# Performance work log

Measured on AMD Instinct MI355X. Metric: run time of the kernel, lower is better.

## Reference

```python
import jax, jax.numpy as jnp
import numpy as np

EPS = 1e-6  # config.model.train_hparams.eps
DIM_MODEL = 512
DIM_K = 64  # dim_q = dim_k = dim_v


def setup_inputs() -> dict:
    key = jax.random.key(0)
    ks = jax.random.split(key, 10)
    B, S = 8, 2048
    query = jax.random.normal(ks[0], (B, S, DIM_MODEL), dtype=jnp.float32)
    key_t = jax.random.normal(ks[1], (B, S, DIM_MODEL), dtype=jnp.float32)
    value = jax.random.normal(ks[2], (B, S, DIM_MODEL), dtype=jnp.float32)
    attention_mask = jax.random.randint(ks[3], (B, S, S), 0, 2, dtype=jnp.int32)
    lim = 1.0 / np.sqrt(DIM_MODEL)
    Wq = jax.random.uniform(ks[4], (DIM_K, DIM_MODEL), jnp.float32, -lim, lim)
    bq = jax.random.uniform(ks[5], (DIM_K,), jnp.float32, -lim, lim)
    Wk = jax.random.uniform(ks[6], (DIM_K, DIM_MODEL), jnp.float32, -lim, lim)
    bk = jax.random.uniform(ks[7], (DIM_K,), jnp.float32, -lim, lim)
    Wv = jax.random.uniform(ks[8], (DIM_K, DIM_MODEL), jnp.float32, -lim, lim)
    bv = jax.random.uniform(ks[9], (DIM_K,), jnp.float32, -lim, lim)
    return {"query": query, "key": key_t, "value": value,
            "attention_mask": attention_mask,
            "Wq": Wq, "bq": bq, "Wk": Wk, "bk": bk, "Wv": Wv, "bv": bv}


def reference(query, key, value, attention_mask, Wq, bq, Wk, bk, Wv, bv):
    scale = DIM_K ** (-0.5)
    q = jnp.einsum('bsm,dm->bsd', query, Wq) + bq   # (B,S,dk)
    k = jnp.einsum('bsm,dm->bsd', key, Wk) + bk
    v = jnp.einsum('bsm,dm->bsd', value, Wv) + bv
    qk = jnp.einsum('bqd,bkd->bqk', q, k) * scale   # (B,S,S)
    qk = jnp.where(qk == 0, EPS, qk)                 # masked_fill(qk == 0, eps)
    qk = jnp.where(attention_mask == 0, EPS, qk)     # masked_fill(mask == 0, eps)
    attention_weight = jax.nn.softmax(qk, axis=-1)
    attention = jnp.einsum('bqk,bkd->bqd', attention_weight, v)
    return attention, attention_weight
```

## Files before the change

### kernel.cpp

```cpp
#include <hip/hip_runtime.h>

#define BATCH 8
#define SEQ   2048
#define DM    512
#define DK    64
#define NROW  (BATCH*SEQ)
#define EPSV  1e-6f

typedef _Float16 f16x8 __attribute__((ext_vector_type(8)));
typedef _Float16 f16x4 __attribute__((ext_vector_type(4)));
typedef _Float16 f16x2 __attribute__((ext_vector_type(2)));
typedef float    f32x4 __attribute__((ext_vector_type(4)));

__global__ void wcvt(const float* __restrict__ wq, const float* __restrict__ wk,
                     const float* __restrict__ wv, _Float16* __restrict__ w16) {
    int idx = (blockIdx.x * 256 + threadIdx.x) * 4;
    int z = idx >> 15;
    int off = idx & 32767;
    const float* src = (z == 0) ? wq : ((z == 1) ? wk : wv);
    float4 g = *reinterpret_cast<const float4*>(src + off);
    f16x4 h = { (_Float16)g.x, (_Float16)g.y, (_Float16)g.z, (_Float16)g.w };
    *reinterpret_cast<f16x4*>(w16 + idx) = h;
}

__global__ __launch_bounds__(256) void proj(
    const float* __restrict__ query, const float* __restrict__ key,
    const float* __restrict__ value, const _Float16* __restrict__ w16,
    const float* __restrict__ bq, const float* __restrict__ bk, const float* __restrict__ bv,
    _Float16* __restrict__ q16, _Float16* __restrict__ k16, _Float16* __restrict__ vT16)
{
    __shared__ _Float16 xsh[64][72];

    const int t = threadIdx.x;
    const int wave = t >> 6, lane = t & 63;
    const int n16 = lane & 15, quad = lane >> 4;
    const int z = blockIdx.y;
    const float* in   = (z == 0) ? query : ((z == 1) ? key : value);
    const float* bias = (z == 0) ? bq    : ((z == 1) ? bk  : bv);
    const _Float16* wz = w16 + z * (DK * DM);
    const int row0 = blockIdx.x * 64;

    f32x4 acc[4] = {};

    for (int kk = 0; kk < DM; kk += 64) {
        #pragma unroll
        for (int it = 0; it < 4; ++it) {
            int f = t + it * 256;
            int row = f >> 4, kq = f & 15;
            float4 g = *reinterpret_cast<const float4*>(in + (size_t)(row0 + row) * DM + kk + kq * 4);
            f16x4 h = { (_Float16)g.x, (_Float16)g.y, (_Float16)g.z, (_Float16)g.w };
            *reinterpret_cast<f16x4*>(&xsh[row][kq * 4]) = h;
        }
        __syncthreads();
        f16x8 a0 = *reinterpret_cast<const f16x8*>(&xsh[wave * 16 + n16][quad * 8]);
        f16x8 a1 = *reinterpret_cast<const f16x8*>(&xsh[wave * 16 + n16][32 + quad * 8]);
        #pragma unroll
        for (int nt = 0; nt < 4; ++nt) {
            const _Float16* bbase = wz + (size_t)(nt * 16 + n16) * DM + kk + quad * 8;
            f16x8 b0 = *reinterpret_cast<const f16x8*>(bbase);
            f16x8 b1 = *reinterpret_cast<const f16x8*>(bbase + 32);
            acc[nt] = __builtin_amdgcn_mfma_f32_16x16x32_f16(a0, b0, acc[nt], 0, 0, 0);
            acc[nt] = __builtin_amdgcn_mfma_f32_16x16x32_f16(a1, b1, acc[nt], 0, 0, 0);
        }
        __syncthreads();
    }

    const int batch = row0 >> 11, row0s = row0 & (SEQ - 1);
    if (z < 2) {
        _Float16* out = (z == 0) ? q16 : k16;
        #pragma unroll
        for (int nt = 0; nt < 4; ++nt) {
            float bzv = bias[nt * 16 + n16];
            #pragma unroll
            for (int r = 0; r < 4; ++r) {
                int grow = row0 + wave * 16 + quad * 4 + r;
                out[(size_t)grow * DK + nt * 16 + n16] = (_Float16)(acc[nt][r] + bzv);
            }
        }
    } else {
        #pragma unroll
        for (int nt = 0; nt < 4; ++nt) {
            float bzv = bias[nt * 16 + n16];
            f16x4 h = { (_Float16)(acc[nt][0] + bzv), (_Float16)(acc[nt][1] + bzv),
                        (_Float16)(acc[nt][2] + bzv), (_Float16)(acc[nt][3] + bzv) };
            int d = nt * 16 + n16;
            int sbase = row0s + wave * 16 + quad * 4;
            *reinterpret_cast<f16x4*>(vT16 + ((size_t)(batch * DK + d)) * SEQ + sbase) = h;
        }
    }
}

#define RTILE 8
#define SCP   2064

__global__ __launch_bounds__(256, 2) void attn(
    const _Float16* __restrict__ q16,
    const _Float16* __restrict__ k16,
    const _Float16* __restrict__ vT16,
    const int* __restrict__ mask,
    float* __restrict__ attno,
    float* __restrict__ aw)
{
    __shared__ float sc[RTILE][SCP];
    __shared__ _Float16 psh[16][72];
    __shared__ float st_il[RTILE];

    const int t = threadIdx.x;
    const int wave = t >> 6, lane = t & 63;
    const int n16 = lane & 15, quad = lane >> 4;
    const int row0 = blockIdx.x * RTILE;
    const int batch = row0 >> 11, row0s = row0 & (SEQ - 1);

    for (int i = t; i < 16 * 36; i += 256) ((float*)psh)[i] = 0.0f;

    {
        const _Float16* qb = q16 + (size_t)(row0 + n16) * DK + quad * 8;
        f16x8 aq0 = *reinterpret_cast<const f16x8*>(qb);
        f16x8 aq1 = *reinterpret_cast<const f16x8*>(qb + 32);
        for (int c = 0; c < 32; ++c) {
            int key = c * 64 + wave * 16 + n16;
            const _Float16* kb = k16 + (size_t)(batch * SEQ + key) * DK + quad * 8;
            f16x8 b0 = *reinterpret_cast<const f16x8*>(kb);
            f16x8 b1 = *reinterpret_cast<const f16x8*>(kb + 32);
            f32x4 acc = {};
            acc = __builtin_amdgcn_mfma_f32_16x16x32_f16(aq0, b0, acc, 0, 0, 0);
            acc = __builtin_amdgcn_mfma_f32_16x16x32_f16(aq1, b1, acc, 0, 0, 0);
            if (quad < 2) {
                int col = c * 64 + wave * 16 + n16;
                #pragma unroll
                for (int r = 0; r < 4; ++r)
                    sc[quad * 4 + r][col] = acc[r] * 0.125f;
            }
        }
    }
    __syncthreads();

    #pragma unroll
    for (int rr = 0; rr < 2; ++rr) {
        int row = wave * 2 + rr;
        const int4* mrow = reinterpret_cast<const int4*>(
            mask + (size_t)batch * SEQ * SEQ + (size_t)(row0s + row) * SEQ);
        float vmax = -3.4e38f;
        #pragma unroll
        for (int it = 0; it < 8; ++it) {
            int j = it * 64 + lane;
            int4  m4 = mrow[j];
            float4 s4 = *reinterpret_cast<float4*>(&sc[row][j * 4]);
            s4.x = (m4.x == 0 || s4.x == 0.0f) ? EPSV : s4.x;
            s4.y = (m4.y == 0 || s4.y == 0.0f) ? EPSV : s4.y;
            s4.z = (m4.z == 0 || s4.z == 0.0f) ? EPSV : s4.z;
            s4.w = (m4.w == 0 || s4.w == 0.0f) ? EPSV : s4.w;
            *reinterpret_cast<float4*>(&sc[row][j * 4]) = s4;
            vmax = fmaxf(vmax, fmaxf(fmaxf(s4.x, s4.y), fmaxf(s4.z, s4.w)));
        }
        #pragma unroll
        for (int off = 32; off; off >>= 1) vmax = fmaxf(vmax, __shfl_xor(vmax, off));
        float vsum = 0.0f;
        #pragma unroll
        for (int it = 0; it < 8; ++it) {
            int j = it * 64 + lane;
            float4 s4 = *reinterpret_cast<float4*>(&sc[row][j * 4]);
            float4 e4 = { __expf(s4.x - vmax), __expf(s4.y - vmax),
                          __expf(s4.z - vmax), __expf(s4.w - vmax) };
            *reinterpret_cast<float4*>(&sc[row][j * 4]) = e4;
            vsum += (e4.x + e4.y) + (e4.z + e4.w);
        }
        #pragma unroll
        for (int off = 32; off; off >>= 1) vsum += __shfl_xor(vsum, off);
        if (lane == 0) st_il[row] = 1.0f / vsum;
    }
    __syncthreads();

    f32x4 oacc = {};
    const int rowp = t >> 5;
    const int col2 = (t & 31) * 2;
    const float il = st_il[rowp];
    float* awrow = aw + (size_t)batch * SEQ * SEQ + (size_t)(row0s + rowp) * SEQ;
    for (int c = 0; c < 32; ++c) {
        int kk = c * 64;
        const _Float16* vb = vT16 + ((size_t)(batch * DK + wave * 16 + n16)) * SEQ + kk + quad * 8;
        f16x8 bv0 = *reinterpret_cast<const f16x8*>(vb);
        f16x8 bv1 = *reinterpret_cast<const f16x8*>(vb + 32);
        float2 e2 = *reinterpret_cast<float2*>(&sc[rowp][kk + col2]);
        float2 p2 = { e2.x * il, e2.y * il };
        *reinterpret_cast<float2*>(awrow + kk + col2) = p2;
        f16x2 ph = { (_Float16)p2.x, (_Float16)p2.y };
        *reinterpret_cast<f16x2*>(&psh[rowp][col2]) = ph;
        __syncthreads();
        f16x8 ap0 = *reinterpret_cast<const f16x8*>(&psh[n16][quad * 8]);
        f16x8 ap1 = *reinterpret_cast<const f16x8*>(&psh[n16][32 + quad * 8]);
        oacc = __builtin_amdgcn_mfma_f32_16x16x32_f16(ap0, bv0, oacc, 0, 0, 0);
        oacc = __builtin_amdgcn_mfma_f32_16x16x32_f16(ap1, bv1, oacc, 0, 0, 0);
        __syncthreads();
    }
    if (quad < 2) {
        #pragma unroll
        for (int r = 0; r < 4; ++r) {
            int grow = row0 + quad * 4 + r;
            attno[(size_t)grow * DK + wave * 16 + n16] = oacc[r];
        }
    }
}

extern "C" void kernel_launch(void* const* d_in, const int* in_sizes, int n_in,
                              void* d_out, int out_size, void* d_ws, size_t ws_size,
                              hipStream_t stream) {
    const float* query = (const float*)d_in[0];
    const float* key   = (const float*)d_in[1];
    const float* value = (const float*)d_in[2];
    const int*   amask = (const int*)d_in[3];
    const float* Wq = (const float*)d_in[4];
    const float* bq = (const float*)d_in[5];
    const float* Wk = (const float*)d_in[6];
    const float* bk = (const float*)d_in[7];
    const float* Wv = (const float*)d_in[8];
    const float* bv = (const float*)d_in[9];

    float* attno = (float*)d_out;
    float* aw    = attno + (size_t)NROW * DK;

    char* ws = (char*)d_ws;
    _Float16* q16  = (_Float16*)(ws);
    _Float16* k16  = (_Float16*)(ws + (size_t)2097152);
    _Float16* vT16 = (_Float16*)(ws + (size_t)4194304);
    _Float16* w16  = (_Float16*)(ws + (size_t)6291456);

    wcvt<<<96, 256, 0, stream>>>(Wq, Wk, Wv, w16);
    proj<<<dim3(NROW / 64, 3), 256, 0, stream>>>(query, key, value, w16,
                                                 bq, bk, bv, q16, k16, vT16);
    attn<<<NROW / RTILE, 256, 0, stream>>>(q16, k16, vT16, amask, attno, aw);
}
```

Before: 419.9 us.

## Use 16-row fp16 score tiles in attention and drop per-chunk barriers in PV

The attention kernel now handles 16 query rows per block, so every row of the 16x16 MFMA tile is used. Scores are stored in LDS as fp16, which halves shared memory. The softmax keeps values in registers and writes the normalized weights directly. The PV product reads unnormalized fp16 exponentials straight from LDS without any per-chunk syncthreads, and normalizes at output time; K and V fragments are also prefetched one chunk ahead. The V-transpose store in proj goes through LDS so global writes are coalesced. Storing scores and exponentials in fp16 costs precision in the attention weights and output.

```diff
diff --git a/kernel.cpp b/kernel.cpp
--- a/kernel.cpp
+++ b/kernel.cpp
@@ -11,6 +11,8 @@
 typedef _Float16 f16x4 __attribute__((ext_vector_type(4)));
 typedef _Float16 f16x2 __attribute__((ext_vector_type(2)));
 typedef float    f32x4 __attribute__((ext_vector_type(4)));
+
+#define MFMA16(a,b,c) __builtin_amdgcn_mfma_f32_16x16x32_f16(a, b, c, 0, 0, 0)
 
 __global__ void wcvt(const float* __restrict__ wq, const float* __restrict__ wk,
                      const float* __restrict__ wv, _Float16* __restrict__ w16) {
@@ -59,8 +61,8 @@
             const _Float16* bbase = wz + (size_t)(nt * 16 + n16) * DM + kk + quad * 8;
             f16x8 b0 = *reinterpret_cast<const f16x8*>(bbase);
             f16x8 b1 = *reinterpret_cast<const f16x8*>(bbase + 32);
-            acc[nt] = __builtin_amdgcn_mfma_f32_16x16x32_f16(a0, b0, acc[nt], 0, 0, 0);
-            acc[nt] = __builtin_amdgcn_mfma_f32_16x16x32_f16(a1, b1, acc[nt], 0, 0, 0);
+            acc[nt] = MFMA16(a0, b0, acc[nt]);
+            acc[nt] = MFMA16(a1, b1, acc[nt]);
         }
         __syncthreads();
     }
@@ -81,17 +83,23 @@
         #pragma unroll
         for (int nt = 0; nt < 4; ++nt) {
             float bzv = bias[nt * 16 + n16];
-            f16x4 h = { (_Float16)(acc[nt][0] + bzv), (_Float16)(acc[nt][1] + bzv),
-                        (_Float16)(acc[nt][2] + bzv), (_Float16)(acc[nt][3] + bzv) };
-            int d = nt * 16 + n16;
-            int sbase = row0s + wave * 16 + quad * 4;
-            *reinterpret_cast<f16x4*>(vT16 + ((size_t)(batch * DK + d)) * SEQ + sbase) = h;
-        }
-    }
-}
-
-#define RTILE 8
-#define SCP   2064
+            #pragma unroll
+            for (int r = 0; r < 4; ++r)
+                xsh[nt * 16 + n16][wave * 16 + quad * 4 + r] = (_Float16)(acc[nt][r] + bzv);
+        }
+        __syncthreads();
+        int d = t >> 2, s0 = (t & 3) * 16;
+        _Float16* dst = vT16 + ((size_t)(batch * DK + d)) * SEQ + row0s + s0;
+        f16x8 h0, h1;
+        #pragma unroll
+        for (int j = 0; j < 8; ++j) { h0[j] = xsh[d][s0 + j]; h1[j] = xsh[d][s0 + 8 + j]; }
+        *reinterpret_cast<f16x8*>(dst)     = h0;
+        *reinterpret_cast<f16x8*>(dst + 8) = h1;
+    }
+}
+
+#define RT  16
+#define SCH 2056
 
 __global__ __launch_bounds__(256, 2) void attn(
     const _Float16* __restrict__ q16,
@@ -101,57 +109,60 @@
     float* __restrict__ attno,
     float* __restrict__ aw)
 {
-    __shared__ float sc[RTILE][SCP];
-    __shared__ _Float16 psh[16][72];
-    __shared__ float st_il[RTILE];
+    __shared__ _Float16 sc[RT][SCH];
+    __shared__ float st_il[RT];
 
     const int t = threadIdx.x;
     const int wave = t >> 6, lane = t & 63;
     const int n16 = lane & 15, quad = lane >> 4;
-    const int row0 = blockIdx.x * RTILE;
+    const int row0 = blockIdx.x * RT;
     const int batch = row0 >> 11, row0s = row0 & (SEQ - 1);
-
-    for (int i = t; i < 16 * 36; i += 256) ((float*)psh)[i] = 0.0f;
 
     {
         const _Float16* qb = q16 + (size_t)(row0 + n16) * DK + quad * 8;
         f16x8 aq0 = *reinterpret_cast<const f16x8*>(qb);
         f16x8 aq1 = *reinterpret_cast<const f16x8*>(qb + 32);
+        const _Float16* kbase = k16 + (size_t)(batch * SEQ) * DK;
+        const _Float16* kb = kbase + (size_t)(wave * 16 + n16) * DK + quad * 8;
+        f16x8 b0 = *reinterpret_cast<const f16x8*>(kb);
+        f16x8 b1 = *reinterpret_cast<const f16x8*>(kb + 32);
         for (int c = 0; c < 32; ++c) {
-            int key = c * 64 + wave * 16 + n16;
-            const _Float16* kb = k16 + (size_t)(batch * SEQ + key) * DK + quad * 8;
-            f16x8 b0 = *reinterpret_cast<const f16x8*>(kb);
-            f16x8 b1 = *reinterpret_cast<const f16x8*>(kb + 32);
+            f16x8 cb0 = b0, cb1 = b1;
+            if (c < 31) {
+                const _Float16* nb = kbase + (size_t)((c + 1) * 64 + wave * 16 + n16) * DK + quad * 8;
+                b0 = *reinterpret_cast<const f16x8*>(nb);
+                b1 = *reinterpret_cast<const f16x8*>(nb + 32);
+            }
             f32x4 acc = {};
-            acc = __builtin_amdgcn_mfma_f32_16x16x32_f16(aq0, b0, acc, 0, 0, 0);
-            acc = __builtin_amdgcn_mfma_f32_16x16x32_f16(aq1, b1, acc, 0, 0, 0);
-            if (quad < 2) {
-                int col = c * 64 + wave * 16 + n16;
-                #pragma unroll
-                for (int r = 0; r < 4; ++r)
-                    sc[quad * 4 + r][col] = acc[r] * 0.125f;
-            }
+            acc = MFMA16(aq0, cb0, acc);
+            acc = MFMA16(aq1, cb1, acc);
+            int col = c * 64 + wave * 16 + n16;
+            #pragma unroll
+            for (int r = 0; r < 4; ++r)
+                sc[quad * 4 + r][col] = (_Float16)(acc[r] * 0.125f);
         }
     }
     __syncthreads();
 
-    #pragma unroll
-    for (int rr = 0; rr < 2; ++rr) {
-        int row = wave * 2 + rr;
+    #pragma unroll 1
+    for (int rr = 0; rr < 4; ++rr) {
+        int row = wave * 4 + rr;
         const int4* mrow = reinterpret_cast<const int4*>(
             mask + (size_t)batch * SEQ * SEQ + (size_t)(row0s + row) * SEQ);
+        float e[32];
         float vmax = -3.4e38f;
         #pragma unroll
         for (int it = 0; it < 8; ++it) {
             int j = it * 64 + lane;
             int4  m4 = mrow[j];
-            float4 s4 = *reinterpret_cast<float4*>(&sc[row][j * 4]);
-            s4.x = (m4.x == 0 || s4.x == 0.0f) ? EPSV : s4.x;
-            s4.y = (m4.y == 0 || s4.y == 0.0f) ? EPSV : s4.y;
-            s4.z = (m4.z == 0 || s4.z == 0.0f) ? EPSV : s4.z;
-            s4.w = (m4.w == 0 || s4.w == 0.0f) ? EPSV : s4.w;
-            *reinterpret_cast<float4*>(&sc[row][j * 4]) = s4;
-            vmax = fmaxf(vmax, fmaxf(fmaxf(s4.x, s4.y), fmaxf(s4.z, s4.w)));
+            f16x4 s4 = *reinterpret_cast<const f16x4*>(&sc[row][j * 4]);
+            float s0 = (float)s4[0], s1 = (float)s4[1], s2 = (float)s4[2], s3 = (float)s4[3];
+            s0 = (m4.x == 0 || s0 == 0.0f) ? EPSV : s0;
+            s1 = (m4.y == 0 || s1 == 0.0f) ? EPSV : s1;
+            s2 = (m4.z == 0 || s2 == 0.0f) ? EPSV : s2;
+            s3 = (m4.w == 0 || s3 == 0.0f) ? EPSV : s3;
+            e[it * 4 + 0] = s0; e[it * 4 + 1] = s1; e[it * 4 + 2] = s2; e[it * 4 + 3] = s3;
+            vmax = fmaxf(vmax, fmaxf(fmaxf(s0, s1), fmaxf(s2, s3)));
         }
         #pragma unroll
         for (int off = 32; off; off >>= 1) vmax = fmaxf(vmax, __shfl_xor(vmax, off));
@@ -159,45 +170,48 @@
         #pragma unroll
         for (int it = 0; it < 8; ++it) {
             int j = it * 64 + lane;
-            float4 s4 = *reinterpret_cast<float4*>(&sc[row][j * 4]);
-            float4 e4 = { __expf(s4.x - vmax), __expf(s4.y - vmax),
-                          __expf(s4.z - vmax), __expf(s4.w - vmax) };
-            *reinterpret_cast<float4*>(&sc[row][j * 4]) = e4;
-            vsum += (e4.x + e4.y) + (e4.z + e4.w);
+            float e0 = __expf(e[it * 4 + 0] - vmax), e1 = __expf(e[it * 4 + 1] - vmax);
+            float e2 = __expf(e[it * 4 + 2] - vmax), e3 = __expf(e[it * 4 + 3] - vmax);
+            e[it * 4 + 0] = e0; e[it * 4 + 1] = e1; e[it * 4 + 2] = e2; e[it * 4 + 3] = e3;
+            f16x4 h = { (_Float16)e0, (_Float16)e1, (_Float16)e2, (_Float16)e3 };
+            *reinterpret_cast<f16x4*>(&sc[row][j * 4]) = h;
+            vsum += (e0 + e1) + (e2 + e3);
         }
         #pragma unroll
         for (int off = 32; off; off >>= 1) vsum += __shfl_xor(vsum, off);
-        if (lane == 0) st_il[row] = 1.0f / vsum;
+        float il = 1.0f / vsum;
+        if (lane == 0) st_il[row] = il;
+        float* awrow = aw + (size_t)batch * SEQ * SEQ + (size_t)(row0s + row) * SEQ;
+        #pragma unroll
+        for (int it = 0; it < 8; ++it) {
+            int j = it * 64 + lane;
+            float4 p4 = { e[it * 4 + 0] * il, e[it * 4 + 1] * il,
+                          e[it * 4 + 2] * il, e[it * 4 + 3] * il };
+            *reinterpret_cast<float4*>(awrow + j * 4) = p4;
+        }
     }
     __syncthreads();
 
-    f32x4 oacc = {};
-    const int rowp = t >> 5;
-    const int col2 = (t & 31) * 2;
-    const float il = st_il[rowp];
-    float* awrow = aw + (size_t)batch * SEQ * SEQ + (size_t)(row0s + rowp) * SEQ;
-    for (int c = 0; c < 32; ++c) {
-        int kk = c * 64;
-        const _Float16* vb = vT16 + ((size_t)(batch * DK + wave * 16 + n16)) * SEQ + kk + quad * 8;
-        f16x8 bv0 = *reinterpret_cast<const f16x8*>(vb);
-        f16x8 bv1 = *reinterpret_cast<const f16x8*>(vb + 32);
-        float2 e2 = *reinterpret_cast<float2*>(&sc[rowp][kk + col2]);
-        float2 p2 = { e2.x * il, e2.y * il };
-        *reinterpret_cast<float2*>(awrow + kk + col2) = p2;
-        f16x2 ph = { (_Float16)p2.x, (_Float16)p2.y };
-        *reinterpret_cast<f16x2*>(&psh[rowp][col2]) = ph;
-        __syncthreads();
-        f16x8 ap0 = *reinterpret_cast<const f16x8*>(&psh[n16][quad * 8]);
-        f16x8 ap1 = *reinterpret_cast<const f16x8*>(&psh[n16][32 + quad * 8]);
-        oacc = __builtin_amdgcn_mfma_f32_16x16x32_f16(ap0, bv0, oacc, 0, 0, 0);
-        oacc = __builtin_amdgcn_mfma_f32_16x16x32_f16(ap1, bv1, oacc, 0, 0, 0);
-        __syncthreads();
-    }
-    if (quad < 2) {
+    {
+        f32x4 oacc = {};
+        const _Float16* vbase = vT16 + ((size_t)(batch * DK + wave * 16 + n16)) * SEQ;
+        f16x8 bv0 = *reinterpret_cast<const f16x8*>(vbase + quad * 8);
+        f16x8 bv1 = *reinterpret_cast<const f16x8*>(vbase + 32 + quad * 8);
+        for (int c = 0; c < 32; ++c) {
+            f16x8 cb0 = bv0, cb1 = bv1;
+            if (c < 31) {
+                bv0 = *reinterpret_cast<const f16x8*>(vbase + (c + 1) * 64 + quad * 8);
+                bv1 = *reinterpret_cast<const f16x8*>(vbase + (c + 1) * 64 + 32 + quad * 8);
+            }
+            f16x8 a0 = *reinterpret_cast<const f16x8*>(&sc[n16][c * 64 + quad * 8]);
+            f16x8 a1 = *reinterpret_cast<const f16x8*>(&sc[n16][c * 64 + 32 + quad * 8]);
+            oacc = MFMA16(a0, cb0, oacc);
+            oacc = MFMA16(a1, cb1, oacc);
+        }
         #pragma unroll
         for (int r = 0; r < 4; ++r) {
-            int grow = row0 + quad * 4 + r;
-            attno[(size_t)grow * DK + wave * 16 + n16] = oacc[r];
+            int row = quad * 4 + r;
+            attno[(size_t)(row0 + row) * DK + wave * 16 + n16] = oacc[r] * st_il[row];
         }
     }
 }
@@ -228,5 +242,5 @@
     wcvt<<<96, 256, 0, stream>>>(Wq, Wk, Wv, w16);
     proj<<<dim3(NROW / 64, 3), 256, 0, stream>>>(query, key, value, w16,
                                                  bq, bk, bv, q16, k16, vT16);
-    attn<<<NROW / RTILE, 256, 0, stream>>>(q16, k16, vT16, amask, attno, aw);
-}
+    attn<<<NROW / RT, 256, 0, stream>>>(q16, k16, vT16, amask, attno, aw);
+}
```

Result: faster. 378.6 us (-9.8%).
